# Performance work log

Measured on AMD Instinct MI355X. Metric: run time of the kernel, lower is better.

The kernel has to match this reference:

```python
import jax, jax.numpy as jnp
import numpy as np
from jax import lax

D_MODEL = 512
N_BLOCKS = 8
VOCAB = 2048
MEL = 80
D_INNER = 2 * D_MODEL      # standard Mamba expand=2
STATE = 16                 # AudioConstants.MAMBA_STATE_DIM
DT_RANK = D_MODEL // 16    # 32
CONV_K = 4                 # causal depthwise conv kernel
B, T = 4, 2048


def setup_inputs() -> dict:
    key = jax.random.key(0)
    ks = jax.random.split(key, 16)
    s = 0.02
    nb = N_BLOCKS
    inp = {
        "feats": jax.random.normal(ks[0], (B, T, MEL), jnp.float32),
        "feat_lens": jax.random.randint(ks[1], (B,), 0, T, jnp.int32),
        # frontend
        "conv1_w": jax.random.normal(ks[2], (D_MODEL, MEL, 3), jnp.float32) * s,
        "conv1_b": jnp.zeros((D_MODEL,), jnp.float32),
        "conv2_w": jax.random.normal(ks[3], (D_MODEL, D_MODEL, 3), jnp.float32) * s,
        "conv2_b": jnp.zeros((D_MODEL,), jnp.float32),
        # stacked per-block Mamba params (leading dim = n_blocks)
        "norm_w": jnp.ones((nb, D_MODEL), jnp.float32),
        "in_proj_w": jax.random.normal(ks[4], (nb, D_MODEL, 2 * D_INNER), jnp.float32) * s,
        "dwconv_w": jax.random.normal(ks[5], (nb, D_INNER, CONV_K), jnp.float32) * s,
        "dwconv_b": jnp.zeros((nb, D_INNER), jnp.float32),
        "x_proj_w": jax.random.normal(ks[6], (nb, D_INNER, DT_RANK + 2 * STATE), jnp.float32) * s,
        "dt_proj_w": jax.random.normal(ks[7], (nb, DT_RANK, D_INNER), jnp.float32) * s,
        "dt_proj_b": jnp.full((nb, D_INNER), -4.6, jnp.float32),  # softplus(-4.6)~0.01
        "A_log": jnp.tile(jnp.log(jnp.arange(1, STATE + 1, dtype=jnp.float32))[None, None, :], (nb, D_INNER, 1)),
        "Dskip": jnp.ones((nb, D_INNER), jnp.float32),
        "out_proj_w": jax.random.normal(ks[8], (nb, D_INNER, D_MODEL), jnp.float32) * s,
        # CTC head
        "head_w": jax.random.normal(ks[9], (D_MODEL, VOCAB), jnp.float32) * s,
        "head_b": jnp.zeros((VOCAB,), jnp.float32),
    }
    return inp


def _conv1d(x, w, b, stride, pad):
    # x: (B, Cin, L), w: (Cout, Cin, K)
    y = lax.conv_general_dilated(x, w, (stride,), [(pad, pad)],
                                 dimension_numbers=("NCH", "OIH", "NCH"))
    return y + b[None, :, None]


def _mamba_layer(x, p):
    nw, ipw, cw, cb, xpw, dpw, dpb, alog, dsk, opw = p
    res = x
    # RMSNorm
    xn = x * lax.rsqrt(jnp.mean(x * x, axis=-1, keepdims=True) + 1e-5) * nw
    xz = xn @ ipw                                # (B, L, 2*di)
    xs, z = jnp.split(xz, 2, axis=-1)
    # causal depthwise conv over time
    xc = jnp.pad(xs.transpose(0, 2, 1), ((0, 0), (0, 0), (CONV_K - 1, 0)))
    xc = lax.conv_general_dilated(xc, cw[:, None, :], (1,), [(0, 0)],
                                  dimension_numbers=("NCH", "OIH", "NCH"),
                                  feature_group_count=D_INNER)
    xs = jax.nn.silu((xc + cb[None, :, None]).transpose(0, 2, 1))  # (B, L, di)
    # input-dependent SSM params
    xdb = xs @ xpw                               # (B, L, dt_rank + 2N)
    dt, Bm, Cm = jnp.split(xdb, [DT_RANK, DT_RANK + STATE], axis=-1)
    delta = jax.nn.softplus(dt @ dpw + dpb)      # (B, L, di)
    A = -jnp.exp(alog)                           # (di, N)
    dA = jnp.exp(delta[..., None] * A)           # (B, L, di, N)
    dBx = delta[..., None] * Bm[:, :, None, :] * xs[..., None]

    def step(h, inp):
        dA_t, dBx_t, C_t = inp                   # (B,di,N),(B,di,N),(B,N)
        h = dA_t * h + dBx_t
        y = jnp.einsum("bdn,bn->bd", h, C_t)
        return h, y

    h0 = jnp.zeros((x.shape[0], D_INNER, STATE), x.dtype)
    _, ys = lax.scan(step, h0, (dA.transpose(1, 0, 2, 3),
                                dBx.transpose(1, 0, 2, 3),
                                Cm.transpose(1, 0, 2)))
    y = ys.transpose(1, 0, 2) + xs * dsk          # (B, L, di)
    y = y * jax.nn.silu(z)
    return res + y @ opw, None


def reference(feats, feat_lens, conv1_w, conv1_b, conv2_w, conv2_b,
              norm_w, in_proj_w, dwconv_w, dwconv_b, x_proj_w,
              dt_proj_w, dt_proj_b, A_log, Dskip, out_proj_w,
              head_w, head_b):
    x = feats.transpose(0, 2, 1)                  # (B, 80, T)
    x = jax.nn.gelu(_conv1d(x, conv1_w, conv1_b, 2, 1), approximate=False)
    x = jax.nn.gelu(_conv1d(x, conv2_w, conv2_b, 2, 1), approximate=False)
    x = x.transpose(0, 2, 1)                      # (B, T/4, D)
    params = (norm_w, in_proj_w, dwconv_w, dwconv_b, x_proj_w,
              dt_proj_w, dt_proj_b, A_log, Dskip, out_proj_w)
    x, _ = lax.scan(_mamba_layer, x, params)
    logits = x @ head_w + head_b                  # (B, T/4, V)
    out_lens = jnp.maximum(feat_lens // 4, 1)
    return logits, out_lens
```

## Files before the change

kernel.cpp:

```cpp
#include <hip/hip_runtime.h>
#include <hip/hip_bf16.h>

#define DMODEL 512
#define NB 8
#define VOCABSZ 2048
#define MEL 80
#define DIN 1024
#define NSTATE 16
#define DTRANK 32
#define BATCH 4
#define TIN 2048
#define LL1 1024
#define LSEQ 512
#define MROWS (BATCH*LSEQ)
#define M1ROWS (BATCH*LL1)
#define NCHUNK 16
#define LCHUNK 32

typedef unsigned short u16;
typedef unsigned int   u32;
typedef __attribute__((ext_vector_type(8))) short short8;
typedef __attribute__((ext_vector_type(4))) float f32x4;

__device__ __forceinline__ float bf2f(u16 v) { return __uint_as_float(((u32)v) << 16); }
__device__ __forceinline__ u16 f2bf(float f) {
    u32 u = __float_as_uint(f);
    return (u16)((u + 0x7fffu + ((u >> 16) & 1u)) >> 16);
}
__device__ __forceinline__ float gelu_exact(float v) {
    return 0.5f * v * (1.0f + erff(v * 0.70710678118654752f));
}
__device__ __forceinline__ float silu_f(float v) { return v / (1.0f + __expf(-v)); }
__device__ __forceinline__ float softplus_f(float v) { return v > 20.f ? v : log1pf(__expf(v)); }

template<int WM, int WN, int MR, int NR, int EPI, int SPLITK>
__global__ __launch_bounds__(WM*WN*64) void gemm2_bf16(
    const u16* __restrict__ A, int lda,
    const u16* __restrict__ BT, int ldb,
    const float* __restrict__ bias,
    float* __restrict__ Cf, u16* __restrict__ Cb, int ldc,
    int K, int zstride)
{
    constexpr int BM = WM * MR * 16;
    constexpr int BN = WN * NR * 16;
    constexpr int NT = WM * WN * 64;
    constexpr int LA = (BM * 4) / NT;
    constexpr int LB = (BN * 4) / NT;
    __shared__ __align__(16) u16 As[2][BM * 32];
    __shared__ __align__(16) u16 Bs[2][BN * 32];
    const int tid = threadIdx.x;
    const int m0 = blockIdx.y * BM, n0 = blockIdx.x * BN;
    const int lane = tid & 63;
    const int wave = tid >> 6;
    const int wm = wave / WN, wn = wave % WN;
    const int lr = lane & 15, lk = lane >> 4;

    int kt0 = 0, kend = K;
    if (SPLITK > 1) {
        const int kb = K / SPLITK;
        kt0 = blockIdx.z * kb;
        kend = kt0 + kb;
        Cf += (size_t)blockIdx.z * zstride;
    }

    f32x4 acc[MR][NR];
#pragma unroll
    for (int m = 0; m < MR; ++m)
#pragma unroll
        for (int n = 0; n < NR; ++n) acc[m][n] = (f32x4){0.f, 0.f, 0.f, 0.f};

    auto stage = [&](int buf, int kt) {
#pragma unroll
        for (int c = 0; c < LA; ++c) {
            int idx = c * NT + tid;
            const u16* src = A + (size_t)(m0 + (idx >> 2)) * lda + kt + (idx & 3) * 8;
            __builtin_amdgcn_global_load_lds(
                (const __attribute__((address_space(1))) void*)src,
                (__attribute__((address_space(3))) void*)&As[buf][idx * 8], 16, 0, 0);
        }
#pragma unroll
        for (int c = 0; c < LB; ++c) {
            int idx = c * NT + tid;
            const u16* src = BT + (size_t)(n0 + (idx >> 2)) * ldb + kt + (idx & 3) * 8;
            __builtin_amdgcn_global_load_lds(
                (const __attribute__((address_space(1))) void*)src,
                (__attribute__((address_space(3))) void*)&Bs[buf][idx * 8], 16, 0, 0);
        }
    };

    stage(0, kt0);
    __syncthreads();
    int cur = 0;
    for (int kt = kt0; kt < kend; kt += 32) {
        if (kt + 32 < kend) stage(cur ^ 1, kt + 32);
        short8 a[MR], b[NR];
#pragma unroll
        for (int m = 0; m < MR; ++m)
            a[m] = *(const short8*)&As[cur][((wm * MR + m) * 16 + lr) * 32 + lk * 8];
#pragma unroll
        for (int n = 0; n < NR; ++n)
            b[n] = *(const short8*)&Bs[cur][((wn * NR + n) * 16 + lr) * 32 + lk * 8];
#pragma unroll
        for (int m = 0; m < MR; ++m)
#pragma unroll
            for (int n = 0; n < NR; ++n)
                acc[m][n] = __builtin_amdgcn_mfma_f32_16x16x32_bf16(a[m], b[n], acc[m][n], 0, 0, 0);
        __syncthreads();
        cur ^= 1;
    }

#pragma unroll
    for (int m = 0; m < MR; ++m) {
#pragma unroll
        for (int n = 0; n < NR; ++n) {
#pragma unroll
            for (int r = 0; r < 4; ++r) {
                const int row = m0 + (wm * MR + m) * 16 + lk * 4 + r;
                const int col = n0 + (wn * NR + n) * 16 + lr;
                float v = acc[m][n][r];
                if (EPI == 1)      v += bias[col];
                else if (EPI == 2) v = gelu_exact(v + bias[col]);
                else if (EPI == 3) v = softplus_f(v + bias[col]);
                else if (EPI == 4) v += Cf[(size_t)row * ldc + col];
                if (Cf) Cf[(size_t)row * ldc + col] = v;
                if (Cb) Cb[(size_t)row * ldc + col] = f2bf(v);
            }
        }
    }
}

__global__ __launch_bounds__(256) void tcast_k(const float* __restrict__ in, u16* __restrict__ out,
                                               int R, int C, size_t sin, size_t sout) {
    in  += (size_t)blockIdx.z * sin;
    out += (size_t)blockIdx.z * sout;
    __shared__ float s[32][33];
    const int tx = threadIdx.x & 31, ty = threadIdx.x >> 5;
    const int r0 = blockIdx.y * 32, c0 = blockIdx.x * 32;
#pragma unroll
    for (int i = 0; i < 4; ++i)
        s[ty + i * 8][tx] = in[(size_t)(r0 + ty + i * 8) * C + c0 + tx];
    __syncthreads();
#pragma unroll
    for (int i = 0; i < 4; ++i)
        out[(size_t)(c0 + ty + i * 8) * R + r0 + tx] = f2bf(s[tx][ty + i * 8]);
}

__global__ void castpad_k(const float* __restrict__ in, u16* __restrict__ out,
                          int rows, int cin, int cout, int instride,
                          size_t sin, size_t sout) {
    in  += (size_t)blockIdx.z * sin;
    out += (size_t)blockIdx.z * sout;
    int idx = blockIdx.x * 256 + threadIdx.x;
    if (idx >= rows * cout) return;
    int c = idx % cout, r = idx / cout;
    out[idx] = (c < cin) ? f2bf(in[(size_t)r * instride + c]) : (u16)0;
}

__global__ void im2col1_k(const float* __restrict__ feats, u16* __restrict__ out) {
    int idx = blockIdx.x * 256 + threadIdx.x;
    int c = idx & 255, m = idx >> 8;
    int l1 = m & (LL1 - 1), b = m >> 10;
    float v = 0.f;
    if (c < 240) {
        int ci = c / 3, kk = c - ci * 3;
        int t = 2 * l1 - 1 + kk;
        if (t >= 0 && t < TIN) v = feats[((size_t)b * TIN + t) * MEL + ci];
    }
    out[idx] = f2bf(v);
}

__global__ void im2col2_k(const u16* __restrict__ y1b, u16* __restrict__ out) {
    int idx = blockIdx.x * 256 + threadIdx.x;
    int c = idx % 1536, m = idx / 1536;
    int l = m & (LSEQ - 1), b = m >> 9;
    int ci = c / 3, kk = c - ci * 3;
    int t = 2 * l - 1 + kk;
    out[idx] = (t >= 0 && t < LL1) ? y1b[((size_t)b * LL1 + t) * 512 + ci] : (u16)0;
}

__global__ __launch_bounds__(256) void rmsnorm_k(const float* __restrict__ x,
                                                 const float* __restrict__ nw,
                                                 u16* __restrict__ xn) {
    int m = blockIdx.x;
    int tid = threadIdx.x;
    const float2 v = *reinterpret_cast<const float2*>(&x[(size_t)m * DMODEL + tid * 2]);
    float ss = v.x * v.x + v.y * v.y;
#pragma unroll
    for (int o = 32; o > 0; o >>= 1) ss += __shfl_down(ss, o);
    __shared__ float sred[4];
    __shared__ float sscale;
    if ((tid & 63) == 0) sred[tid >> 6] = ss;
    __syncthreads();
    if (tid == 0) {
        float tot = sred[0] + sred[1] + sred[2] + sred[3];
        sscale = rsqrtf(tot / 512.f + 1e-5f);
    }
    __syncthreads();
    float sc = sscale;
    u32 pack = (u32)f2bf(v.x * sc * nw[tid * 2]) | ((u32)f2bf(v.y * sc * nw[tid * 2 + 1]) << 16);
    *reinterpret_cast<u32*>(&xn[(size_t)m * DMODEL + tid * 2]) = pack;
}

__global__ __launch_bounds__(256) void dwconv_silu_k(const u16* __restrict__ xzb,
                                                     const float* __restrict__ cw,
                                                     const float* __restrict__ cb,
                                                     u16* __restrict__ xsb) {
    int d = blockIdx.x * 256 + threadIdx.x;
    int m = blockIdx.y;
    int l = m & (LSEQ - 1);
    int b = m >> 9;
    float acc = cb[d];
    const float4 w4 = *reinterpret_cast<const float4*>(&cw[d * 4]);
    const float wk[4] = {w4.x, w4.y, w4.z, w4.w};
#pragma unroll
    for (int k = 0; k < 4; k++) {
        int t = l - 3 + k;
        if (t >= 0) acc += wk[k] * bf2f(xzb[((size_t)(b * LSEQ + t)) * (2 * DIN) + d]);
    }
    xsb[(size_t)m * DIN + d] = f2bf(silu_f(acc));
}

__global__ void xreduce_k(const float* __restrict__ part, float* __restrict__ xdb,
                          u16* __restrict__ dtb) {
    int i4 = blockIdx.x * 256 + threadIdx.x;
    const float4 p0 = *(const float4*)&part[i4 * 4];
    const float4 p1 = *(const float4*)&part[131072 + i4 * 4];
    const float4 p2 = *(const float4*)&part[262144 + i4 * 4];
    const float4 p3 = *(const float4*)&part[393216 + i4 * 4];
    float4 s;
    s.x = p0.x + p1.x + p2.x + p3.x;
    s.y = p0.y + p1.y + p2.y + p3.y;
    s.z = p0.z + p1.z + p2.z + p3.z;
    s.w = p0.w + p1.w + p2.w + p3.w;
    *(float4*)&xdb[i4 * 4] = s;
    int c4 = i4 & 15, r = i4 >> 4;
    if (c4 < 8) {
        u32 lo = (u32)f2bf(s.x) | ((u32)f2bf(s.y) << 16);
        u32 hi = (u32)f2bf(s.z) | ((u32)f2bf(s.w) << 16);
        *(u32*)&dtb[r * 32 + c4 * 4]     = lo;
        *(u32*)&dtb[r * 32 + c4 * 4 + 2] = hi;
    }
}

template<int PASS>
__global__ __launch_bounds__(256) void scan_chunk_k(
    const u16* __restrict__ deltab, const u16* __restrict__ xsb,
    const float* __restrict__ xdb, const u16* __restrict__ xzb,
    const float* __restrict__ alog, const float* __restrict__ dsk,
    float* __restrict__ P, float* __restrict__ Q,
    u16* __restrict__ yb)
{
    __shared__ float s_bc[LCHUNK * 32];
    __shared__ float s_dl[LCHUNK * 64];
    __shared__ float s_xs[LCHUNK * 64];
    __shared__ float s_z [PASS ? LCHUNK * 64 : 1];

    const int tid  = threadIdx.x;
    const int j    = tid & 3;
    const int dsub = tid >> 2;
    const int d0   = blockIdx.x * 64;
    const int c    = blockIdx.y;
    const int b    = blockIdx.z;
    const int d    = d0 + dsub;
    const size_t rbase = (size_t)b * LSEQ + c * LCHUNK;

    for (int idx = tid; idx < LCHUNK * 32; idx += 256) {
        int t = idx >> 5, cc = idx & 31;
        s_bc[idx] = xdb[(rbase + t) * 64 + 32 + cc];
    }
    for (int idx = tid; idx < LCHUNK * 64; idx += 256) {
        int t = idx >> 6, dd = idx & 63;
        s_dl[idx] = bf2f(deltab[(rbase + t) * DIN + d0 + dd]);
        s_xs[idx] = bf2f(xsb[(rbase + t) * DIN + d0 + dd]);
        if (PASS) s_z[idx] = bf2f(xzb[(rbase + t) * (2 * DIN) + DIN + d0 + dd]);
    }
    __syncthreads();

    float a[4], h[4];
#pragma unroll
    for (int nj = 0; nj < 4; nj++)
        a[nj] = -__expf(alog[(size_t)d * NSTATE + j * 4 + nj]);

    const size_t chstride = (size_t)DIN * NSTATE;
    const size_t chcol = (size_t)d * NSTATE + j * 4;
    h[0] = h[1] = h[2] = h[3] = 0.f;
    if (PASS) {
        for (int c2 = 0; c2 < c; ++c2) {
            const size_t o = ((size_t)(b * NCHUNK + c2)) * chstride + chcol;
            const float4 Pv = *(const float4*)&P[o];
            const float4 Qv = *(const float4*)&Q[o];
            h[0] = fmaf(Pv.x, h[0], Qv.x);
            h[1] = fmaf(Pv.y, h[1], Qv.y);
            h[2] = fmaf(Pv.z, h[2], Qv.z);
            h[3] = fmaf(Pv.w, h[3], Qv.w);
        }
    }
    const float dskv = PASS ? dsk[d] : 0.f;
    float sdl = 0.f;

    for (int t = 0; t < LCHUNK; t++) {
        const float dl = s_dl[t * 64 + dsub];
        const float xv = s_xs[t * 64 + dsub];
        const float dlx = dl * xv;
        if (!PASS) sdl += dl;
        float yv = 0.f;
#pragma unroll
        for (int nj = 0; nj < 4; nj++) {
            const float bn = s_bc[t * 32 + j * 4 + nj];
            const float dA = __expf(dl * a[nj]);
            h[nj] = fmaf(dA, h[nj], dlx * bn);
            if (PASS) {
                const float cn = s_bc[t * 32 + 16 + j * 4 + nj];
                yv = fmaf(h[nj], cn, yv);
            }
        }
        if (PASS) {
            yv += __shfl_xor(yv, 1);
            yv += __shfl_xor(yv, 2);
            if (j == 0) {
                const float zv = s_z[t * 64 + dsub];
                yb[(rbase + t) * DIN + d] = f2bf((yv + xv * dskv) * silu_f(zv));
            }
        }
    }

    if (!PASS) {
        const size_t o = ((size_t)(b * NCHUNK + c)) * chstride + chcol;
        float4 Pv, Qv;
        Pv.x = __expf(a[0] * sdl); Pv.y = __expf(a[1] * sdl);
        Pv.z = __expf(a[2] * sdl); Pv.w = __expf(a[3] * sdl);
        Qv.x = h[0]; Qv.y = h[1]; Qv.z = h[2]; Qv.w = h[3];
        *(float4*)&P[o] = Pv;
        *(float4*)&Q[o] = Qv;
    }
}

__global__ void lens_k(const int* __restrict__ feat_lens, float* __restrict__ out) {
    int b = threadIdx.x;
    if (b < BATCH) {
        int v = feat_lens[b] / 4;
        if (v < 1) v = 1;
        out[b] = (float)v;
    }
}

extern "C" void kernel_launch(void* const* d_in, const int* in_sizes, int n_in,
                              void* d_out, int out_size, void* d_ws, size_t ws_size,
                              hipStream_t stream)
{
    const float* feats = (const float*)d_in[0];
    const int*   flens = (const int*)  d_in[1];
    const float* c1w = (const float*)d_in[2];
    const float* c1b = (const float*)d_in[3];
    const float* c2w = (const float*)d_in[4];
    const float* c2b = (const float*)d_in[5];
    const float* nw  = (const float*)d_in[6];
    const float* ipw = (const float*)d_in[7];
    const float* cw  = (const float*)d_in[8];
    const float* cb  = (const float*)d_in[9];
    const float* xpw = (const float*)d_in[10];
    const float* dpw = (const float*)d_in[11];
    const float* dpb = (const float*)d_in[12];
    const float* alog= (const float*)d_in[13];
    const float* dskp= (const float*)d_in[14];
    const float* opw = (const float*)d_in[15];
    const float* hw  = (const float*)d_in[16];
    const float* hb  = (const float*)d_in[17];

    float* ws = (float*)d_ws;
    u16*  XZb    = (u16*)ws;
    float* X     = ws + 2097152;
    u16*  XN     = (u16*)(ws + 3145728);
    u16*  Xb     = (u16*)(ws + 3670016);
    u16*  XSb    = (u16*)(ws + 4194304);
    u16*  DELb   = (u16*)(ws + 5242880);
    float* XDB   = ws + 6291456;
    float* P     = ws + 6422528;
    u16*  dtb    = (u16*)(ws + 7471104);
    u16*  Yb     = (u16*)(ws + 7503872);
    float* XDBp  = ws + 8552448;
    u16*  ipwTa  = (u16*)(ws + 9076736);
    u16*  opwTa  = (u16*)(ws + 13271040);
    u16*  hwT    = (u16*)(ws + 15368192);
    u16*  xpwT   = (u16*)(ws + 15892480);
    u16*  dpwT   = (u16*)(ws + 16154624);
    u16*  c1wb   = (u16*)(ws + 16285696);
    u16*  c2wb   = (u16*)(ws + 16351232);
    u16*  Y1b    = (u16*)(ws + 16744448);
    float* logits = (float*)d_out;
    float* Q     = logits;

    castpad_k<<<dim3(512, 1, 1), 256, 0, stream>>>(c1w, c1wb, 512, 240, 256, 240, 0, 0);
    castpad_k<<<dim3(3072, 1, 1), 256, 0, stream>>>(c2w, c2wb, 512, 1536, 1536, 1536, 0, 0);
    tcast_k<<<dim3(64, 16, 1), 256, 0, stream>>>(hw, hwT, 512, 2048, 0, 0);
    tcast_k<<<dim3(2, 32, 8), 256, 0, stream>>>(xpw, xpwT, 1024, 64, 65536, 65536);
    tcast_k<<<dim3(32, 1, 8), 256, 0, stream>>>(dpw, dpwT, 32, 1024, 32768, 32768);
    tcast_k<<<dim3(64, 16, 8), 256, 0, stream>>>(ipw, ipwTa, 512, 2048, 1048576, 1048576);
    tcast_k<<<dim3(16, 32, 8), 256, 0, stream>>>(opw, opwTa, 1024, 512, 524288, 524288);

    im2col1_k<<<4096, 256, 0, stream>>>(feats, XZb);
    gemm2_bf16<2, 2, 4, 2, 2, 1><<<dim3(8, 32), 256, 0, stream>>>(
        XZb, 256, c1wb, 256, c1b, nullptr, Y1b, 512, 256, 0);
    im2col2_k<<<12288, 256, 0, stream>>>(Y1b, XZb);
    gemm2_bf16<2, 2, 2, 2, 2, 1><<<dim3(8, 32), 256, 0, stream>>>(
        XZb, 1536, c2wb, 1536, c2b, X, nullptr, 512, 1536, 0);

    for (int blk = 0; blk < NB; ++blk) {
        rmsnorm_k<<<MROWS, 256, 0, stream>>>(X, nw + blk * DMODEL, XN);
        gemm2_bf16<2, 2, 4, 2, 0, 1><<<dim3(32, 16), 256, 0, stream>>>(
            XN, 512, ipwTa + (size_t)blk * 1048576, 512, nullptr,
            nullptr, XZb, 2048, 512, 0);
        dwconv_silu_k<<<dim3(4, MROWS), 256, 0, stream>>>(
            XZb, cw + blk * DIN * 4, cb + blk * DIN, XSb);
        gemm2_bf16<2, 2, 2, 2, 0, 4><<<dim3(1, 32, 4), 256, 0, stream>>>(
            XSb, 1024, xpwT + (size_t)blk * 65536, 1024, nullptr,
            XDBp, nullptr, 64, 1024, 131072);
        xreduce_k<<<128, 256, 0, stream>>>(XDBp, XDB, dtb);
        gemm2_bf16<2, 2, 4, 2, 3, 1><<<dim3(16, 16), 256, 0, stream>>>(
            dtb, 32, dpwT + (size_t)blk * 32768, 32, dpb + blk * DIN,
            nullptr, DELb, 1024, 32, 0);
        scan_chunk_k<0><<<dim3(16, NCHUNK, BATCH), 256, 0, stream>>>(
            DELb, XSb, XDB, nullptr, alog + (size_t)blk * DIN * NSTATE,
            nullptr, P, Q, nullptr);
        scan_chunk_k<1><<<dim3(16, NCHUNK, BATCH), 256, 0, stream>>>(
            DELb, XSb, XDB, XZb, alog + (size_t)blk * DIN * NSTATE,
            dskp + blk * DIN, P, Q, Yb);
        gemm2_bf16<2, 2, 2, 2, 4, 1><<<dim3(8, 32), 256, 0, stream>>>(
            Yb, 1024, opwTa + (size_t)blk * 524288, 1024, nullptr,
            X, Xb, 512, 1024, 0);
    }

    gemm2_bf16<2, 2, 4, 2, 1, 1><<<dim3(32, 16), 256, 0, stream>>>(
        Xb, 512, hwT, 512, hb, logits, nullptr, 2048, 512, 0);
    lens_k<<<1, 64, 0, stream>>>(flens, logits + (size_t)MROWS * VOCABSZ);
}
```

Measured before the change: 858.6 us.

## Fuse x_proj reduction with dt_proj, fold lens into im2col, retile GEMMs

Replaces the x_proj split-K reduction kernel and the small dt_proj GEMM with a single kernel. It sums the partials, keeps the dt slice in LDS, and computes softplus(dt@W+b) with scalar FMAs, removing one launch and a round trip through the intermediate per block. The lens computation is folded into im2col1, and the in_proj and head GEMMs use a wider tile with half the grid. The scalar dt_proj loses tensor-core use, and the wider tiles reduce the number of workgroups.

Result: slower. 1.011 ms (+17.8%).

```diff
diff --git a/kernel.cpp b/kernel.cpp
--- a/kernel.cpp
+++ b/kernel.cpp
@@ -7,7 +7,6 @@
 #define MEL 80
 #define DIN 1024
 #define NSTATE 16
-#define DTRANK 32
 #define BATCH 4
 #define TIN 2048
 #define LL1 1024
@@ -156,8 +155,14 @@
     out[idx] = (c < cin) ? f2bf(in[(size_t)r * instride + c]) : (u16)0;
 }
 
-__global__ void im2col1_k(const float* __restrict__ feats, u16* __restrict__ out) {
+__global__ void im2col1_k(const float* __restrict__ feats, u16* __restrict__ out,
+                          const int* __restrict__ feat_lens, float* __restrict__ lens_out) {
     int idx = blockIdx.x * 256 + threadIdx.x;
+    if (blockIdx.x == 0 && threadIdx.x < BATCH) {
+        int v = feat_lens[threadIdx.x] / 4;
+        if (v < 1) v = 1;
+        lens_out[threadIdx.x] = (float)v;
+    }
     int c = idx & 255, m = idx >> 8;
     int l1 = m & (LL1 - 1), b = m >> 10;
     float v = 0.f;
@@ -220,25 +225,48 @@
     xsb[(size_t)m * DIN + d] = f2bf(silu_f(acc));
 }
 
-__global__ void xreduce_k(const float* __restrict__ part, float* __restrict__ xdb,
-                          u16* __restrict__ dtb) {
-    int i4 = blockIdx.x * 256 + threadIdx.x;
-    const float4 p0 = *(const float4*)&part[i4 * 4];
-    const float4 p1 = *(const float4*)&part[131072 + i4 * 4];
-    const float4 p2 = *(const float4*)&part[262144 + i4 * 4];
-    const float4 p3 = *(const float4*)&part[393216 + i4 * 4];
-    float4 s;
-    s.x = p0.x + p1.x + p2.x + p3.x;
-    s.y = p0.y + p1.y + p2.y + p3.y;
-    s.z = p0.z + p1.z + p2.z + p3.z;
-    s.w = p0.w + p1.w + p2.w + p3.w;
-    *(float4*)&xdb[i4 * 4] = s;
-    int c4 = i4 & 15, r = i4 >> 4;
-    if (c4 < 8) {
-        u32 lo = (u32)f2bf(s.x) | ((u32)f2bf(s.y) << 16);
-        u32 hi = (u32)f2bf(s.z) | ((u32)f2bf(s.w) << 16);
-        *(u32*)&dtb[r * 32 + c4 * 4]     = lo;
-        *(u32*)&dtb[r * 32 + c4 * 4 + 2] = hi;
+__global__ __launch_bounds__(256) void xdt_k(const float* __restrict__ part,
+                                             const u16* __restrict__ dpwT,
+                                             const float* __restrict__ dpb,
+                                             float* __restrict__ xdb,
+                                             u16* __restrict__ delb) {
+    __shared__ float dt_lds[16][32];
+    const int tid = threadIdx.x;
+    const int r0 = blockIdx.x * 16;
+#pragma unroll
+    for (int half = 0; half < 2; ++half) {
+        int idx = half * 256 + tid;
+        int r = idx >> 5, c = idx & 31;
+        size_t o = (size_t)(r0 + r) * 64 + c;
+        float dtv = part[o] + part[131072 + o] + part[262144 + o] + part[393216 + o];
+        dt_lds[r][c] = dtv;
+        size_t o2 = o + 32;
+        float bcv = part[o2] + part[131072 + o2] + part[262144 + o2] + part[393216 + o2];
+        xdb[(size_t)(r0 + r) * 64 + 32 + c] = bcv;
+    }
+    __syncthreads();
+#pragma unroll
+    for (int i = 0; i < 4; ++i) {
+        const int dcol = i * 256 + tid;
+        const uint4 w0 = *(const uint4*)&dpwT[dcol * 32];
+        const uint4 w1 = *(const uint4*)&dpwT[dcol * 32 + 8];
+        const uint4 w2 = *(const uint4*)&dpwT[dcol * 32 + 16];
+        const uint4 w3 = *(const uint4*)&dpwT[dcol * 32 + 24];
+        float wk[32];
+        const u32 wa[16] = {w0.x, w0.y, w0.z, w0.w, w1.x, w1.y, w1.z, w1.w,
+                            w2.x, w2.y, w2.z, w2.w, w3.x, w3.y, w3.z, w3.w};
+#pragma unroll
+        for (int k = 0; k < 16; ++k) {
+            wk[2 * k]     = bf2f((u16)(wa[k] & 0xffffu));
+            wk[2 * k + 1] = bf2f((u16)(wa[k] >> 16));
+        }
+        const float bias = dpb[dcol];
+        for (int r = 0; r < 16; ++r) {
+            float acc = bias;
+#pragma unroll
+            for (int k = 0; k < 32; ++k) acc = fmaf(dt_lds[r][k], wk[k], acc);
+            delb[(size_t)(r0 + r) * DIN + dcol] = f2bf(softplus_f(acc));
+        }
     }
 }
 
@@ -332,15 +360,6 @@
         Qv.x = h[0]; Qv.y = h[1]; Qv.z = h[2]; Qv.w = h[3];
         *(float4*)&P[o] = Pv;
         *(float4*)&Q[o] = Qv;
-    }
-}
-
-__global__ void lens_k(const int* __restrict__ feat_lens, float* __restrict__ out) {
-    int b = threadIdx.x;
-    if (b < BATCH) {
-        int v = feat_lens[b] / 4;
-        if (v < 1) v = 1;
-        out[b] = (float)v;
     }
 }
 
@@ -376,7 +395,6 @@
     u16*  DELb   = (u16*)(ws + 5242880);
     float* XDB   = ws + 6291456;
     float* P     = ws + 6422528;
-    u16*  dtb    = (u16*)(ws + 7471104);
     u16*  Yb     = (u16*)(ws + 7503872);
     float* XDBp  = ws + 8552448;
     u16*  ipwTa  = (u16*)(ws + 9076736);
@@ -398,7 +416,7 @@
     tcast_k<<<dim3(64, 16, 8), 256, 0, stream>>>(ipw, ipwTa, 512, 2048, 1048576, 1048576);
     tcast_k<<<dim3(16, 32, 8), 256, 0, stream>>>(opw, opwTa, 1024, 512, 524288, 524288);
 
-    im2col1_k<<<4096, 256, 0, stream>>>(feats, XZb);
+    im2col1_k<<<4096, 256, 0, stream>>>(feats, XZb, flens, logits + (size_t)MROWS * VOCABSZ);
     gemm2_bf16<2, 2, 4, 2, 2, 1><<<dim3(8, 32), 256, 0, stream>>>(
         XZb, 256, c1wb, 256, c1b, nullptr, Y1b, 512, 256, 0);
     im2col2_k<<<12288, 256, 0, stream>>>(Y1b, XZb);
@@ -407,7 +425,7 @@
 
     for (int blk = 0; blk < NB; ++blk) {
         rmsnorm_k<<<MROWS, 256, 0, stream>>>(X, nw + blk * DMODEL, XN);
-        gemm2_bf16<2, 2, 4, 2, 0, 1><<<dim3(32, 16), 256, 0, stream>>>(
+        gemm2_bf16<2, 2, 4, 4, 0, 1><<<dim3(16, 16), 256, 0, stream>>>(
             XN, 512, ipwTa + (size_t)blk * 1048576, 512, nullptr,
             nullptr, XZb, 2048, 512, 0);
         dwconv_silu_k<<<dim3(4, MROWS), 256, 0, stream>>>(
@@ -415,10 +433,8 @@
         gemm2_bf16<2, 2, 2, 2, 0, 4><<<dim3(1, 32, 4), 256, 0, stream>>>(
             XSb, 1024, xpwT + (size_t)blk * 65536, 1024, nullptr,
             XDBp, nullptr, 64, 1024, 131072);
-        xreduce_k<<<128, 256, 0, stream>>>(XDBp, XDB, dtb);
-        gemm2_bf16<2, 2, 4, 2, 3, 1><<<dim3(16, 16), 256, 0, stream>>>(
-            dtb, 32, dpwT + (size_t)blk * 32768, 32, dpb + blk * DIN,
-            nullptr, DELb, 1024, 32, 0);
+        xdt_k<<<128, 256, 0, stream>>>(XDBp, dpwT + (size_t)blk * 32768,
+                                       dpb + blk * DIN, XDB, DELb);
         scan_chunk_k<0><<<dim3(16, NCHUNK, BATCH), 256, 0, stream>>>(
             DELb, XSb, XDB, nullptr, alog + (size_t)blk * DIN * NSTATE,
             nullptr, P, Q, nullptr);
@@ -430,7 +446,6 @@
             X, Xb, 512, 1024, 0);
     }
 
-    gemm2_bf16<2, 2, 4, 2, 1, 1><<<dim3(32, 16), 256, 0, stream>>>(
+    gemm2_bf16<2, 2, 4, 4, 1, 1><<<dim3(16, 16), 256, 0, stream>>>(
         Xb, 512, hwT, 512, hb, logits, nullptr, 2048, 512, 0);
-    lens_k<<<1, 64, 0, stream>>>(flens, logits + (size_t)MROWS * VOCABSZ);
-}
+}
```
